# Performance work log

Hardware: AMD Instinct MI355X
Metric: run time of the kernel (lower is better)

## Reference

```python
import jax, jax.numpy as jnp
import numpy as np
from jax import lax

B, L, H, KSIZE = 8, 16384, 128, 65
PAD = KSIZE // 2  # 32; odd kernel keeps output length == L


def setup_inputs() -> dict:
    key = jax.random.key(0)
    kq, kk, kv, kw = jax.random.split(key, 4)
    Q = jax.random.normal(kq, (B, L, H), dtype=jnp.float32)
    K = jax.random.normal(kk, (B, L, H), dtype=jnp.float32)
    V = jax.random.normal(kv, (B, L, H), dtype=jnp.float32)
    # Conv1d weight [out_ch, in_ch, kernel], kaiming-like scale
    W = jax.random.normal(kw, (H, H, KSIZE), dtype=jnp.float32) / np.sqrt(H * KSIZE)
    return {"Q": Q, "K": K, "V": V, "W": W}


def reference(Q, K, V, W):
    # [B, L, H] -> [B, H, L] (channels-first, matching torch transpose(1,2))
    Qt = jnp.swapaxes(Q, 1, 2)
    Kt = jnp.swapaxes(K, 1, 2)
    Vt = jnp.swapaxes(V, 1, 2)
    # Conv1d over sequence dim; lax conv is cross-correlation like torch
    conv_q = lax.conv_general_dilated(
        Qt, W,
        window_strides=(1,),
        padding=[(PAD, PAD)],
        dimension_numbers=("NCH", "OIH", "NCH"),
    )  # [B, H, L]
    scores = conv_q * Kt                      # elementwise gate
    A = jax.nn.softmax(scores, axis=-1)       # softmax over sequence dim
    Z = A * Vt                                # weighted V (elementwise)
    return jnp.swapaxes(Z, 1, 2)              # back to [B, L, H]
```

## Files before the change

### kernel.cpp

```cpp
#include <hip/hip_runtime.h>
#include <stdint.h>

#define BATCH 8
#define LSEQ 16384
#define HDIM 128
#define KSZ 65
#define PADW 32
#define LH (LSEQ*HDIM)
#define TL 256
#define NROWS (TL + 2*PADW)
#define LBLKS (LSEQ/TL)
#define EXP_SHIFT 20.0f
#define SLOT 16384

#define WS_WBF_OFF 4096

typedef __attribute__((ext_vector_type(8))) short bf16x8;
typedef __attribute__((ext_vector_type(4))) short bf16x4;
typedef __attribute__((ext_vector_type(16))) float f32x16;

__device__ __forceinline__ unsigned short f2bf(float f) {
  unsigned int u = __float_as_uint(f);
  return (unsigned short)((u + 0x7FFFu + ((u >> 16) & 1u)) >> 16);
}

__global__ __launch_bounds__(256) void wcvt_kernel(const float* __restrict__ W,
                                                   unsigned short* __restrict__ Wbf) {
  __shared__ float lw[KSZ*HDIM];
  const int o = blockIdx.x;
  const float* src = W + (size_t)o * (HDIM*KSZ);
  for (int t = threadIdx.x; t < HDIM*KSZ; t += 256) lw[t] = src[t];
  __syncthreads();
  const int ob  = o >> 5;
  const int l31 = o & 31;
  for (int idx = threadIdx.x; idx < KSZ*HDIM; idx += 256) {
    const int k = idx >> 7;
    const int i = idx & 127;
    const int kk  = i >> 4;
    const int hi2 = (i >> 3) & 1;
    const int e   = i & 7;
    const size_t dst = (size_t)k*SLOT + kk*2048 + ob*512 + hi2*256 + l31*8 + e;
    Wbf[dst] = f2bf(lw[i*KSZ + k]);
  }
}

__device__ __forceinline__ void stage_tap(const unsigned short* __restrict__ gsrc,
                                          char* lbase, int w, int lane) {
  const char* gb = (const char*)gsrc;
#pragma unroll
  for (int r = 0; r < 4; ++r) {
    const int off = r*8192 + w*1024;
    __builtin_amdgcn_global_load_lds(
        (const __attribute__((address_space(1))) unsigned int*)(gb + off + lane*16),
        (__attribute__((address_space(3))) unsigned int*)(lbase + off),
        16, 0, 0);
  }
}

__global__ __launch_bounds__(512, 2) void conv_gate_kernel(
    const float* __restrict__ Qm, const float* __restrict__ Km,
    const unsigned short* __restrict__ Wfrag,
    float* __restrict__ Eout, float* __restrict__ gsum) {

  __shared__ __align__(16) char smem[147456];
  unsigned short* Qs = (unsigned short*)smem;
  char* WsBase = smem + 81920;

  const int tid  = threadIdx.x;
  const int lane = tid & 63;
  const int w    = tid >> 6;
  const int ks   = w & 1;
  const int wc   = (w >> 1) & 1;
  const int wr   = w >> 2;
  const int l31  = lane & 31;
  const int hi2  = lane >> 5;

  const int bx = blockIdx.x;
  const int b  = bx >> 6;
  const int l0 = (bx & 63) << 8;

  {
    const int r0 = tid >> 5;
    const int c4 = (tid & 31) << 2;
    const float* qbase = Qm + (size_t)b*LH + c4;
#pragma unroll
    for (int it = 0; it < NROWS/16; ++it) {
      const int r = it*16 + r0;
      const int grow = l0 - PADW + r;
      bf16x4 pk = {0, 0, 0, 0};
      if (grow >= 0 && grow < LSEQ) {
        const float4 qv = *(const float4*)(qbase + (size_t)grow*HDIM);
        pk[0] = (short)f2bf(qv.x); pk[1] = (short)f2bf(qv.y);
        pk[2] = (short)f2bf(qv.z); pk[3] = (short)f2bf(qv.w);
      }
      *(bf16x4*)(&Qs[r*HDIM + (c4 ^ ((r & 15) << 3))]) = pk;
    }
  }

  stage_tap(Wfrag, WsBase, w, lane);

  f32x16 acc[4][2] = {};

  __syncthreads();

  const int arow0 = wr*128 + l31;
  const int bbase = wc*1024 + lane*8;

#define LOADC(c, A, B) { \
    const int i0 = (ks*64 + (c)*16 + hi2*8) ^ xa; \
    A[0] = *(const bf16x8*)(&Qs[(rb     )*HDIM + i0]); \
    A[1] = *(const bf16x8*)(&Qs[(rb + 32)*HDIM + i0]); \
    A[2] = *(const bf16x8*)(&Qs[(rb + 64)*HDIM + i0]); \
    A[3] = *(const bf16x8*)(&Qs[(rb + 96)*HDIM + i0]); \
    B[0] = *(const bf16x8*)(&slot[(ks*4 + (c))*2048 + bbase]); \
    B[1] = *(const bf16x8*)(&slot[(ks*4 + (c))*2048 + bbase + 512]); \
  }
#define MM(A, B) \
    acc[0][0] = __builtin_amdgcn_mfma_f32_32x32x16_bf16(A[0], B[0], acc[0][0], 0, 0, 0); \
    acc[0][1] = __builtin_amdgcn_mfma_f32_32x32x16_bf16(A[0], B[1], acc[0][1], 0, 0, 0); \
    acc[1][0] = __builtin_amdgcn_mfma_f32_32x32x16_bf16(A[1], B[0], acc[1][0], 0, 0, 0); \
    acc[1][1] = __builtin_amdgcn_mfma_f32_32x32x16_bf16(A[1], B[1], acc[1][1], 0, 0, 0); \
    acc[2][0] = __builtin_amdgcn_mfma_f32_32x32x16_bf16(A[2], B[0], acc[2][0], 0, 0, 0); \
    acc[2][1] = __builtin_amdgcn_mfma_f32_32x32x16_bf16(A[2], B[1], acc[2][1], 0, 0, 0); \
    acc[3][0] = __builtin_amdgcn_mfma_f32_32x32x16_bf16(A[3], B[0], acc[3][0], 0, 0, 0); \
    acc[3][1] = __builtin_amdgcn_mfma_f32_32x32x16_bf16(A[3], B[1], acc[3][1], 0, 0, 0);

  for (int k = 0; k < KSZ; ++k) {
    const unsigned short* slot = (const unsigned short*)(WsBase + (k & 1)*32768);
    const int rb = k + arow0;
    const int xa = (rb & 15) << 3;

    {
      bf16x8 A0[4], B0[2], A1[4], B1[2];
      LOADC(0, A0, B0)
      LOADC(1, A1, B1)
      if (k < KSZ-1)
        stage_tap(Wfrag + (size_t)(k+1)*SLOT, WsBase + ((k+1) & 1)*32768, w, lane);
      __builtin_amdgcn_s_barrier();
      asm volatile("s_waitcnt lgkmcnt(0)" ::: "memory");
      __builtin_amdgcn_sched_barrier(0);
      __builtin_amdgcn_s_setprio(1);
      MM(A0, B0)
      MM(A1, B1)
      __builtin_amdgcn_s_setprio(0);
      __builtin_amdgcn_s_barrier();
    }
    {
      bf16x8 A0[4], B0[2], A1[4], B1[2];
      LOADC(2, A0, B0)
      LOADC(3, A1, B1)
      __builtin_amdgcn_s_barrier();
      asm volatile("s_waitcnt lgkmcnt(0)" ::: "memory");
      __builtin_amdgcn_sched_barrier(0);
      __builtin_amdgcn_s_setprio(1);
      MM(A0, B0)
      MM(A1, B1)
      __builtin_amdgcn_s_setprio(0);
      asm volatile("s_waitcnt vmcnt(0)" ::: "memory");
      __builtin_amdgcn_s_barrier();
    }
  }
#undef LOADC
#undef MM

  float* red = (float*)smem;
  const int widx = wr*2 + wc;
  float* reg = red + widx*8192 + lane*4;
  if (ks == 1) {
#pragma unroll
    for (int e4 = 0; e4 < 32; ++e4) {
      const int mfr = e4 >> 3, nf = (e4 >> 2) & 1, r4 = (e4 & 3) << 2;
      float4 v;
      v.x = acc[mfr][nf][r4];   v.y = acc[mfr][nf][r4+1];
      v.z = acc[mfr][nf][r4+2]; v.w = acc[mfr][nf][r4+3];
      *(float4*)(reg + e4*256) = v;
    }
  }
  __syncthreads();

  if (ks == 0) {
#pragma unroll
    for (int e4 = 0; e4 < 32; ++e4) {
      const int mfr = e4 >> 3, nf = (e4 >> 2) & 1, r4 = (e4 & 3) << 2;
      const float4 v = *(const float4*)(reg + e4*256);
      acc[mfr][nf][r4]   += v.x; acc[mfr][nf][r4+1] += v.y;
      acc[mfr][nf][r4+2] += v.z; acc[mfr][nf][r4+3] += v.w;
    }
    float psum[2] = {0.f, 0.f};
#pragma unroll
    for (int mfr = 0; mfr < 4; ++mfr) {
#pragma unroll
      for (int r = 0; r < 16; ++r) {
        const int row = wr*128 + mfr*32 + (r & 3) + 8*(r >> 2) + 4*hi2;
        const size_t gb = (size_t)b*LH + (size_t)(l0 + row)*HDIM + wc*64 + l31;
#pragma unroll
        for (int nf = 0; nf < 2; ++nf) {
          const float s = acc[mfr][nf][r] * Km[gb + nf*32];
          const float e = __expf(s - EXP_SHIFT);
          Eout[gb + nf*32] = e;
          psum[nf] += e;
        }
      }
    }
    psum[0] += __shfl_xor(psum[0], 32);
    psum[1] += __shfl_xor(psum[1], 32);
    if (hi2 == 0) {
      atomicAdd(&gsum[b*HDIM + wc*64 + l31],      psum[0]);
      atomicAdd(&gsum[b*HDIM + wc*64 + 32 + l31], psum[1]);
    }
  }
}

__global__ __launch_bounds__(256) void finalize_kernel(float* __restrict__ out,
                                                       const float* __restrict__ V,
                                                       const float* __restrict__ gsum) {
  const int total4 = (BATCH*LH) >> 2;
  const int stride = gridDim.x * blockDim.x;
  for (int f = blockIdx.x*blockDim.x + threadIdx.x; f < total4; f += stride) {
    const float4 e = ((const float4*)out)[f];
    const float4 v = ((const float4*)V)[f];
    const int e0 = f << 2;
    const float* gs = gsum + ((e0 >> 21) << 7) + (e0 & 127);
    float4 z;
    z.x = e.x * v.x / gs[0];
    z.y = e.y * v.y / gs[1];
    z.z = e.z * v.z / gs[2];
    z.w = e.w * v.w / gs[3];
    ((float4*)out)[f] = z;
  }
}

extern "C" void kernel_launch(void* const* d_in, const int* in_sizes, int n_in,
                              void* d_out, int out_size, void* d_ws, size_t ws_size,
                              hipStream_t stream) {
  (void)in_sizes; (void)n_in; (void)out_size; (void)ws_size;
  const float* Q = (const float*)d_in[0];
  const float* K = (const float*)d_in[1];
  const float* V = (const float*)d_in[2];
  const float* W = (const float*)d_in[3];
  float* out  = (float*)d_out;
  float* gsum = (float*)d_ws;
  unsigned short* Wbf = (unsigned short*)((char*)d_ws + WS_WBF_OFF);

  hipMemsetAsync(d_ws, 0, BATCH*HDIM*sizeof(float), stream);
  wcvt_kernel<<<HDIM, 256, 0, stream>>>(W, Wbf);
  conv_gate_kernel<<<BATCH*LBLKS, 512, 0, stream>>>(Q, K, Wbf, out, gsum);
  finalize_kernel<<<2048, 256, 0, stream>>>(out, V, gsum);
}
```

Before: 288.0 us.

## Split weight taps into half-slots with triple-buffered prefetch two phases ahead

Splits each conv tap's weight slab into two half-slots (64 input channels each) and streams them through a 3-slot LDS ring, prefetching two phases ahead with vmcnt(2) waits instead of draining all loads each tap. Each phase does one barrier pair instead of two per tap, and the LDS footprint shrinks from 144KB to 128KB. The intent is deeper overlap of the weight global->LDS loads with MFMA work and fewer full drains. The cost is more loop iterations and a finer-grained, less forgiving synchronisation scheme.

```diff
diff --git a/kernel.cpp b/kernel.cpp
--- a/kernel.cpp
+++ b/kernel.cpp
@@ -11,7 +11,8 @@
 #define NROWS (TL + 2*PADW)
 #define LBLKS (LSEQ/TL)
 #define EXP_SHIFT 20.0f
-#define SLOT 16384
+#define HSLOT 8192
+#define NPH (2*KSZ)
 
 #define WS_WBF_OFF 4096
 
@@ -36,19 +37,20 @@
   for (int idx = threadIdx.x; idx < KSZ*HDIM; idx += 256) {
     const int k = idx >> 7;
     const int i = idx & 127;
-    const int kk  = i >> 4;
+    const int hk  = i >> 6;
+    const int kq  = (i >> 4) & 3;
     const int hi2 = (i >> 3) & 1;
     const int e   = i & 7;
-    const size_t dst = (size_t)k*SLOT + kk*2048 + ob*512 + hi2*256 + l31*8 + e;
+    const size_t dst = (size_t)(k*2 + hk)*HSLOT + kq*2048 + ob*512 + hi2*256 + l31*8 + e;
     Wbf[dst] = f2bf(lw[i*KSZ + k]);
   }
 }
 
-__device__ __forceinline__ void stage_tap(const unsigned short* __restrict__ gsrc,
-                                          char* lbase, int w, int lane) {
+__device__ __forceinline__ void stage_half(const unsigned short* __restrict__ gsrc,
+                                           char* lbase, int w, int lane) {
   const char* gb = (const char*)gsrc;
 #pragma unroll
-  for (int r = 0; r < 4; ++r) {
+  for (int r = 0; r < 2; ++r) {
     const int off = r*8192 + w*1024;
     __builtin_amdgcn_global_load_lds(
         (const __attribute__((address_space(1))) unsigned int*)(gb + off + lane*16),
@@ -62,7 +64,7 @@
     const unsigned short* __restrict__ Wfrag,
     float* __restrict__ Eout, float* __restrict__ gsum) {
 
-  __shared__ __align__(16) char smem[147456];
+  __shared__ __align__(16) char smem[131072];
   unsigned short* Qs = (unsigned short*)smem;
   char* WsBase = smem + 81920;
 
@@ -78,6 +80,9 @@
   const int bx = blockIdx.x;
   const int b  = bx >> 6;
   const int l0 = (bx & 63) << 8;
+
+  stage_half(Wfrag,         WsBase,         w, lane);
+  stage_half(Wfrag + HSLOT, WsBase + 16384, w, lane);
 
   {
     const int r0 = tid >> 5;
@@ -97,23 +102,21 @@
     }
   }
 
-  stage_tap(Wfrag, WsBase, w, lane);
-
   f32x16 acc[4][2] = {};
 
   __syncthreads();
 
   const int arow0 = wr*128 + l31;
-  const int bbase = wc*1024 + lane*8;
+  const int bB = wc*1024 + hi2*256 + l31*8;
 
 #define LOADC(c, A, B) { \
-    const int i0 = (ks*64 + (c)*16 + hi2*8) ^ xa; \
+    const int i0 = (hk*64 + ks*32 + (c)*16 + hi2*8) ^ xa; \
     A[0] = *(const bf16x8*)(&Qs[(rb     )*HDIM + i0]); \
     A[1] = *(const bf16x8*)(&Qs[(rb + 32)*HDIM + i0]); \
     A[2] = *(const bf16x8*)(&Qs[(rb + 64)*HDIM + i0]); \
     A[3] = *(const bf16x8*)(&Qs[(rb + 96)*HDIM + i0]); \
-    B[0] = *(const bf16x8*)(&slot[(ks*4 + (c))*2048 + bbase]); \
-    B[1] = *(const bf16x8*)(&slot[(ks*4 + (c))*2048 + bbase + 512]); \
+    B[0] = *(const bf16x8*)(&slot[(ks*2 + (c))*2048 + bB]); \
+    B[1] = *(const bf16x8*)(&slot[(ks*2 + (c))*2048 + bB + 512]); \
   }
 #define MM(A, B) \
     acc[0][0] = __builtin_amdgcn_mfma_f32_32x32x16_bf16(A[0], B[0], acc[0][0], 0, 0, 0); \
@@ -125,40 +128,38 @@
     acc[3][0] = __builtin_amdgcn_mfma_f32_32x32x16_bf16(A[3], B[0], acc[3][0], 0, 0, 0); \
     acc[3][1] = __builtin_amdgcn_mfma_f32_32x32x16_bf16(A[3], B[1], acc[3][1], 0, 0, 0);
 
-  for (int k = 0; k < KSZ; ++k) {
-    const unsigned short* slot = (const unsigned short*)(WsBase + (k & 1)*32768);
+  int scur = 0;
+  const unsigned short* gstage = Wfrag + 2*HSLOT;
+
+  for (int p = 0; p < NPH; ++p) {
+    const int k  = p >> 1;
+    const int hk = p & 1;
+    const unsigned short* slot = (const unsigned short*)(WsBase + scur*16384);
     const int rb = k + arow0;
     const int xa = (rb & 15) << 3;
 
-    {
-      bf16x8 A0[4], B0[2], A1[4], B1[2];
-      LOADC(0, A0, B0)
-      LOADC(1, A1, B1)
-      if (k < KSZ-1)
-        stage_tap(Wfrag + (size_t)(k+1)*SLOT, WsBase + ((k+1) & 1)*32768, w, lane);
-      __builtin_amdgcn_s_barrier();
-      asm volatile("s_waitcnt lgkmcnt(0)" ::: "memory");
-      __builtin_amdgcn_sched_barrier(0);
-      __builtin_amdgcn_s_setprio(1);
-      MM(A0, B0)
-      MM(A1, B1)
-      __builtin_amdgcn_s_setprio(0);
-      __builtin_amdgcn_s_barrier();
-    }
-    {
-      bf16x8 A0[4], B0[2], A1[4], B1[2];
-      LOADC(2, A0, B0)
-      LOADC(3, A1, B1)
-      __builtin_amdgcn_s_barrier();
-      asm volatile("s_waitcnt lgkmcnt(0)" ::: "memory");
-      __builtin_amdgcn_sched_barrier(0);
-      __builtin_amdgcn_s_setprio(1);
-      MM(A0, B0)
-      MM(A1, B1)
-      __builtin_amdgcn_s_setprio(0);
-      asm volatile("s_waitcnt vmcnt(0)" ::: "memory");
-      __builtin_amdgcn_s_barrier();
-    }
+    bf16x8 A0[4], B0[2], A1[4], B1[2];
+    LOADC(0, A0, B0)
+    LOADC(1, A1, B1)
+
+    if (p + 2 < NPH) {
+      const int snxt = (scur == 0) ? 2 : scur - 1;
+      stage_half(gstage, WsBase + snxt*16384, w, lane);
+      gstage += HSLOT;
+    }
+
+    __builtin_amdgcn_sched_barrier(0);
+    __builtin_amdgcn_s_barrier();
+    asm volatile("s_waitcnt lgkmcnt(0)" ::: "memory");
+    __builtin_amdgcn_sched_barrier(0);
+    __builtin_amdgcn_s_setprio(1);
+    MM(A0, B0)
+    MM(A1, B1)
+    __builtin_amdgcn_s_setprio(0);
+    if (p < NPH - 2) asm volatile("s_waitcnt vmcnt(2)" ::: "memory");
+    else             asm volatile("s_waitcnt vmcnt(0)" ::: "memory");
+    __builtin_amdgcn_s_barrier();
+    scur = (scur == 2) ? 0 : scur + 1;
   }
 #undef LOADC
 #undef MM
```

Measured after the change: 304.0 us. +5.6%, slower.

## Software-pipeline Q fragment loads across taps with register double-buffering

Applied to the files above, without the earlier changes.

Restructures the tap loop so A fragments (Q rows) for the next tap are loaded from LDS into a second register set while the current tap's MFMAs run, interleaving B loads with MFMA issue. It drops the per-chunk s_barrier/lgkmcnt waits and setprio sections, keeping one vmcnt wait and barrier per tap. This hides LDS latency and cuts barrier count, but doubles A-fragment register use (32 bf16x8 vectors), which risks spills or lower occupancy under launch_bounds(512,2).

```diff
diff --git a/kernel.cpp b/kernel.cpp
--- a/kernel.cpp
+++ b/kernel.cpp
@@ -106,14 +106,19 @@
   const int arow0 = wr*128 + l31;
   const int bbase = wc*1024 + lane*8;
 
-#define LOADC(c, A, B) { \
-    const int i0 = (ks*64 + (c)*16 + hi2*8) ^ xa; \
-    A[0] = *(const bf16x8*)(&Qs[(rb     )*HDIM + i0]); \
-    A[1] = *(const bf16x8*)(&Qs[(rb + 32)*HDIM + i0]); \
-    A[2] = *(const bf16x8*)(&Qs[(rb + 64)*HDIM + i0]); \
-    A[3] = *(const bf16x8*)(&Qs[(rb + 96)*HDIM + i0]); \
-    B[0] = *(const bf16x8*)(&slot[(ks*4 + (c))*2048 + bbase]); \
-    B[1] = *(const bf16x8*)(&slot[(ks*4 + (c))*2048 + bbase + 512]); \
+#define LOADA(D, KK, c) { \
+    const int rb_ = (KK) + arow0; \
+    const int xa_ = (rb_ & 15) << 3; \
+    const int i0_ = (ks*64 + (c)*16 + hi2*8) ^ xa_; \
+    D[0] = *(const bf16x8*)(&Qs[(rb_     )*HDIM + i0_]); \
+    D[1] = *(const bf16x8*)(&Qs[(rb_ + 32)*HDIM + i0_]); \
+    D[2] = *(const bf16x8*)(&Qs[(rb_ + 64)*HDIM + i0_]); \
+    D[3] = *(const bf16x8*)(&Qs[(rb_ + 96)*HDIM + i0_]); \
+  }
+#define LOADB(B, c) { \
+    const unsigned short* bp_ = slot + (ks*4 + (c))*2048 + bbase; \
+    B[0] = *(const bf16x8*)(bp_); \
+    B[1] = *(const bf16x8*)(bp_ + 512); \
   }
 #define MM(A, B) \
     acc[0][0] = __builtin_amdgcn_mfma_f32_32x32x16_bf16(A[0], B[0], acc[0][0], 0, 0, 0); \
@@ -125,42 +130,37 @@
     acc[3][0] = __builtin_amdgcn_mfma_f32_32x32x16_bf16(A[3], B[0], acc[3][0], 0, 0, 0); \
     acc[3][1] = __builtin_amdgcn_mfma_f32_32x32x16_bf16(A[3], B[1], acc[3][1], 0, 0, 0);
 
-  for (int k = 0; k < KSZ; ++k) {
-    const unsigned short* slot = (const unsigned short*)(WsBase + (k & 1)*32768);
-    const int rb = k + arow0;
-    const int xa = (rb & 15) << 3;
-
-    {
-      bf16x8 A0[4], B0[2], A1[4], B1[2];
-      LOADC(0, A0, B0)
-      LOADC(1, A1, B1)
-      if (k < KSZ-1)
-        stage_tap(Wfrag + (size_t)(k+1)*SLOT, WsBase + ((k+1) & 1)*32768, w, lane);
-      __builtin_amdgcn_s_barrier();
-      asm volatile("s_waitcnt lgkmcnt(0)" ::: "memory");
-      __builtin_amdgcn_sched_barrier(0);
-      __builtin_amdgcn_s_setprio(1);
-      MM(A0, B0)
-      MM(A1, B1)
-      __builtin_amdgcn_s_setprio(0);
-      __builtin_amdgcn_s_barrier();
-    }
-    {
-      bf16x8 A0[4], B0[2], A1[4], B1[2];
-      LOADC(2, A0, B0)
-      LOADC(3, A1, B1)
-      __builtin_amdgcn_s_barrier();
-      asm volatile("s_waitcnt lgkmcnt(0)" ::: "memory");
-      __builtin_amdgcn_sched_barrier(0);
-      __builtin_amdgcn_s_setprio(1);
-      MM(A0, B0)
-      MM(A1, B1)
-      __builtin_amdgcn_s_setprio(0);
-      asm volatile("s_waitcnt vmcnt(0)" ::: "memory");
-      __builtin_amdgcn_s_barrier();
-    }
-  }
-#undef LOADC
+#define TAPBODY(C0, C1, C2, C3, N0, N1, N2, N3, K) { \
+    const unsigned short* slot = (const unsigned short*)(WsBase + ((K) & 1)*32768); \
+    if ((K) < KSZ-1) \
+      stage_tap(Wfrag + (size_t)((K)+1)*SLOT, WsBase + (((K)+1) & 1)*32768, w, lane); \
+    const int kn = ((K)+1 < KSZ) ? (K)+1 : (K); \
+    bf16x8 B0[2], B1[2], B2[2], B3[2]; \
+    LOADB(B0, 0) \
+    LOADB(B1, 1) \
+    MM(C0, B0)  LOADA(N0, kn, 0) \
+    LOADB(B2, 2) \
+    MM(C1, B1)  LOADA(N1, kn, 1) \
+    LOADB(B3, 3) \
+    MM(C2, B2)  LOADA(N2, kn, 2) \
+    MM(C3, B3)  LOADA(N3, kn, 3) \
+    asm volatile("s_waitcnt vmcnt(0)" ::: "memory"); \
+    __builtin_amdgcn_s_barrier(); \
+  }
+
+  bf16x8 AX0[4], AX1[4], AX2[4], AX3[4];
+  bf16x8 AY0[4], AY1[4], AY2[4], AY3[4];
+
+  LOADA(AX0, 0, 0) LOADA(AX1, 0, 1) LOADA(AX2, 0, 2) LOADA(AX3, 0, 3)
+
+  for (int k = 0; k < KSZ-1; k += 2) {
+    TAPBODY(AX0, AX1, AX2, AX3, AY0, AY1, AY2, AY3, k)
+    TAPBODY(AY0, AY1, AY2, AY3, AX0, AX1, AX2, AX3, k+1)
+  }
+  TAPBODY(AX0, AX1, AX2, AX3, AY0, AY1, AY2, AY3, KSZ-1)
+#undef TAPBODY
+#undef LOADA
+#undef LOADB
 #undef MM
 
   float* red = (float*)smem;
```

Result: faster. 278.8 us (-3.2%).
